# Kernel optimization log

Measured on AMD Instinct MI355X. Metric: run time of the kernel, lower is better.

## Reference

```python
import jax, jax.numpy as jnp
import numpy as np
from functools import partial

T = 4
V_TH = 1.0
EPS = 1e-12

# ATan surrogate spike function (spikingjelly surrogate.ATan, alpha=2.0).
# Forward: heaviside(v - v_th). Backward: g * alpha/2 / (1 + (pi/2*alpha*u)^2)
# with alpha=2 -> g / (1 + (pi*u)^2), u = v - v_th.
@jax.custom_vjp
def spike_fn(u):
    return (u >= 0.0).astype(u.dtype)

def _spike_fwd(u):
    return spike_fn(u), u

def _spike_bwd(u, g):
    pi = jnp.asarray(np.pi, dtype=u.dtype)
    return (g / (1.0 + (pi * u) ** 2),)

spike_fn.defvjp(_spike_fwd, _spike_bwd)


def setup_inputs() -> dict:
    key = jax.random.key(0)
    k1, = jax.random.split(key, 1)
    x = jax.random.normal(k1, (4096, 8192), dtype=jnp.float32)
    scale = jnp.asarray(1.5, dtype=jnp.float32)  # activation_scale parameter
    return {"x": x, "scale": scale}


def reference(x, scale):
    safe_scale = jnp.maximum(scale.astype(x.dtype), EPS)
    x_norm = jax.nn.relu(x) / safe_scale  # constant per-step input

    # IFNode, v_reset=None (subtractive reset), v_threshold=1, step_mode='m':
    # v <- v + x; spike = H(v - 1); v <- v - spike * v_th
    def step(v, _):
        v = v + x_norm
        s = spike_fn(v - V_TH)
        v = v - s * V_TH
        return v, s

    v0 = jnp.zeros_like(x_norm)
    _, spikes = jax.lax.scan(step, v0, None, length=T)  # [T, B, D]
    rate = spikes.mean(axis=0)
    return rate * safe_scale
```

## Files before the change

### kernel.cpp

```cpp
#include <hip/hip_runtime.h>


#define THREADS 256
#define UNROLL 8

typedef float f32x4 __attribute__((ext_vector_type(4)));

__device__ __forceinline__ float lif_elem(float x, float safe_scale) {
    float c = fmaxf(x, 0.0f) / safe_scale;
    float v = 0.0f;
    float cnt = 0.0f;
#pragma unroll
    for (int t = 0; t < 4; ++t) {
        v += c;
        float s = ((v - 1.0f) >= 0.0f) ? 1.0f : 0.0f;
        v -= s;
        cnt += s;
    }
    return (cnt * 0.25f) * safe_scale;
}

__device__ __forceinline__ f32x4 lif_vec(f32x4 xv, float ss) {
    f32x4 ov;
    ov.x = lif_elem(xv.x, ss);
    ov.y = lif_elem(xv.y, ss);
    ov.z = lif_elem(xv.z, ss);
    ov.w = lif_elem(xv.w, ss);
    return ov;
}

__global__ __launch_bounds__(THREADS) void lif_kernel(const f32x4* __restrict__ x,
                                                      const float* __restrict__ scale_p,
                                                      f32x4* __restrict__ out,
                                                      int n4) {
    const float ss = fmaxf(scale_p[0], 1e-12f);
    const int nth = gridDim.x * THREADS;
    int i = blockIdx.x * THREADS + threadIdx.x;

    for (; i + (UNROLL - 1) * nth < n4; i += UNROLL * nth) {
        f32x4 xv[UNROLL];
#pragma unroll
        for (int u = 0; u < UNROLL; ++u) {
            xv[u] = x[i + u * nth];
        }
#pragma unroll
        for (int u = 0; u < UNROLL; ++u) {
            f32x4 ov = lif_vec(xv[u], ss);
            __builtin_nontemporal_store(ov, &out[i + u * nth]);
        }
    }
    for (; i < n4; i += nth) {
        f32x4 ov = lif_vec(x[i], ss);
        __builtin_nontemporal_store(ov, &out[i]);
    }
}

__global__ void lif_tail_kernel(const float* __restrict__ x,
                                const float* __restrict__ scale_p,
                                float* __restrict__ out,
                                int start, int n) {
    int idx = start + blockIdx.x * blockDim.x + threadIdx.x;
    if (idx >= n) return;
    float safe_scale = fmaxf(scale_p[0], 1e-12f);
    out[idx] = lif_elem(x[idx], safe_scale);
}

extern "C" void kernel_launch(void* const* d_in, const int* in_sizes, int n_in,
                              void* d_out, int out_size, void* d_ws, size_t ws_size,
                              hipStream_t stream) {
    const float* x = (const float*)d_in[0];
    const float* scale = (const float*)d_in[1];
    float* out = (float*)d_out;
    int n = in_sizes[0];
    int n4 = n >> 2;

    if (n4 > 0) {
        long long per_block = (long long)THREADS * UNROLL;
        int blocks = (int)((n4 + per_block - 1) / per_block);
        if (blocks < 1) blocks = 1;
        lif_kernel<<<blocks, THREADS, 0, stream>>>((const f32x4*)x, scale,
                                                   (f32x4*)out, n4);
    }
    int tail_start = n4 << 2;
    int tail = n - tail_start;
    if (tail > 0) {
        lif_tail_kernel<<<1, 64, 0, stream>>>(x, scale, out, tail_start, n);
    }
}
```

Baseline: 244.1 us.

## Use fixed-size persistent grid with software-prefetched grid-stride loop

```diff
diff --git a/kernel.cpp b/kernel.cpp
--- a/kernel.cpp
+++ b/kernel.cpp
@@ -2,7 +2,7 @@
 
 
 #define THREADS 256
-#define UNROLL 8
+#define BLOCKS 2048
 
 typedef float f32x4 __attribute__((ext_vector_type(4)));
 
@@ -37,22 +37,17 @@
     const int nth = gridDim.x * THREADS;
     int i = blockIdx.x * THREADS + threadIdx.x;
 
-    for (; i + (UNROLL - 1) * nth < n4; i += UNROLL * nth) {
-        f32x4 xv[UNROLL];
-#pragma unroll
-        for (int u = 0; u < UNROLL; ++u) {
-            xv[u] = x[i + u * nth];
-        }
-#pragma unroll
-        for (int u = 0; u < UNROLL; ++u) {
-            f32x4 ov = lif_vec(xv[u], ss);
-            __builtin_nontemporal_store(ov, &out[i + u * nth]);
-        }
+    if (i >= n4) return;
+    int iters = (n4 - 1 - i) / nth + 1;
+
+    f32x4 cur = x[i];
+    for (int k = 0; k < iters - 1; ++k) {
+        f32x4 nxt = x[i + nth];
+        out[i] = lif_vec(cur, ss);
+        cur = nxt;
+        i += nth;
     }
-    for (; i < n4; i += nth) {
-        f32x4 ov = lif_vec(x[i], ss);
-        __builtin_nontemporal_store(ov, &out[i]);
-    }
+    out[i] = lif_vec(cur, ss);
 }
 
 __global__ void lif_tail_kernel(const float* __restrict__ x,
@@ -75,9 +70,9 @@
     int n4 = n >> 2;
 
     if (n4 > 0) {
-        long long per_block = (long long)THREADS * UNROLL;
-        int blocks = (int)((n4 + per_block - 1) / per_block);
-        if (blocks < 1) blocks = 1;
+        int blocks = BLOCKS;
+        long long need = ((long long)n4 + THREADS - 1) / THREADS;
+        if (need < blocks) blocks = (int)need;
         lif_kernel<<<blocks, THREADS, 0, stream>>>((const f32x4*)x, scale,
                                                    (f32x4*)out, n4);
     }
```

Result: faster. 234.2 us (-4.0%).
